# Performance work log

Measured on AMD Instinct MI355X. Metric: run time of the kernel, lower is better.

Reference implementation:

```python
import jax
import jax.numpy as jnp
import numpy as np

# --- dimensions ---
N, B, E, T = 16384, 64, 262144, 1048576   # atoms, molecules, edges, triplets
R, S = 128, 7                              # num_radial, num_spherical
A, EM, TR = 128, 256, 32                   # emb_size_atom, emb_size_edge, emb_size_trip
CRBF, C, BIL, L = 16, 16, 64, 2            # emb_size_rbf, emb_size_cbf, emb_size_bil_trip, num_blocks
NKR, DP = 128, 8                           # num_k_rbf, downprojection_size
CUTOFF, K_CUT, DK = 6.0, 0.4, 0.2


def _k_grid_np():
    ax = np.arange(-2, 3) * DK
    g = np.stack(np.meshgrid(ax, ax, ax, indexing='ij'), -1).reshape(-1, 3)
    nrm = np.linalg.norm(g, axis=1)
    return g[(nrm <= K_CUT + 1e-9) & (nrm > 1e-12)].astype(np.float32)  # [32,3]


def _k_rbf_np(kg):
    nrm = np.linalg.norm(kg, axis=1, keepdims=True)
    centers = np.linspace(0.0, K_CUT, NKR)[None, :]
    gamma = (NKR / K_CUT) ** 2
    return np.exp(-gamma * (nrm - centers) ** 2).astype(np.float32)  # [32,NKR]


def setup_inputs():
    key = jax.random.key(0)
    ks = iter(jax.random.split(key, 48))
    def nrm(shape, fan_in):
        return jax.random.normal(next(ks), shape, jnp.float32) * (fan_in ** -0.5)
    kg_np = _k_grid_np()
    apm = N // B  # atoms per molecule
    mol = jax.random.randint(next(ks), (E,), 0, B)
    inp = {
        'pos': jax.random.uniform(next(ks), (N, 3), jnp.float32) * 5.0,
        'atom_table': jax.random.normal(next(ks), (83, A), jnp.float32),
        'W_edge': nrm((2 * A + R, EM), 2 * A + R), 'b_edge': jnp.zeros((EM,), jnp.float32),
        'W_rbf3': nrm((R, CRBF), R), 'W_rbf3_E': nrm((L, CRBF, EM), CRBF),
        'W_cbf3': nrm((S, R, C), R),
        'W_ba': nrm((L, EM, EM), EM),
        'W_downtrip': nrm((L, EM, TR), EM),
        'W_bil': nrm((L, C, TR, BIL), C * TR),
        'W_up': nrm((L, BIL, EM), BIL),
        'W_res1': nrm((L, EM, EM), EM), 'W_res2': nrm((L, EM, EM), EM),
        'W_rbf_h': nrm((R, CRBF), R), 'W_h': nrm((L, CRBF, EM), CRBF),
        'W_atom': nrm((L, EM, A), EM),
        'k_grid': jnp.asarray(kg_np), 'k_rbf_values': jnp.asarray(_k_rbf_np(kg_np)),
        'W_downk': nrm((NKR, DP), NKR), 'W_kfilter': nrm((DP, A), DP),
        'W_ew': nrm((L, A, A), A),
        'W_cat': nrm((L, 2 * A + EM, EM), 2 * A + EM),
        'W_rbf_out': nrm((R, CRBF), R), 'W_oute': nrm((CRBF, EM), CRBF),
        'W_out1': nrm((EM, A), EM), 'W_out2': nrm((A, 1), A),
        'z': jax.random.randint(next(ks), (N,), 0, 83),
        'edge_src': mol * apm + jax.random.randint(next(ks), (E,), 0, apm),
        'edge_tgt': mol * apm + jax.random.randint(next(ks), (E,), 0, apm),
        'id3_ba': jax.random.randint(next(ks), (T,), 0, E),
        'id3_ca': jax.random.randint(next(ks), (T,), 0, E),
        'batch_idx': jnp.arange(N, dtype=jnp.int32) // apm,
    }
    return inp


def _legendre(x):
    # P_0..P_{S-1}(x) via recurrence
    p = [jnp.ones_like(x), x]
    for l in range(1, S - 1):
        p.append(((2 * l + 1) * x * p[-1] - l * p[-2]) / (l + 1))
    return jnp.stack(p[:S], axis=-1)  # [T,S]


def _forward(pos, atom_table, W_edge, b_edge, W_rbf3, W_rbf3_E, W_cbf3, W_ba,
             W_downtrip, W_bil, W_up, W_res1, W_res2, W_rbf_h, W_h, W_atom,
             k_grid, k_rbf_values, W_downk, W_kfilter, W_ew, W_cat,
             W_rbf_out, W_oute, W_out1, W_out2,
             z, edge_src, edge_tgt, id3_ba, id3_ca, batch_idx):
    seg = lambda x, ids, n: jax.ops.segment_sum(x, ids, num_segments=n)
    silu = jax.nn.silu
    isq2 = 2.0 ** -0.5

    # radial basis (spherical Bessel) with polynomial envelope p=5
    vec = pos[edge_src] - pos[edge_tgt]                       # [E,3]
    d = jnp.sqrt(jnp.sum(vec * vec, -1) + 1e-12)              # [E]
    ds = d / CUTOFF
    env = jnp.where(ds < 1.0, 1.0 - 21.0 * ds**5 + 35.0 * ds**6 - 15.0 * ds**7, 0.0)
    freq = jnp.arange(1, R + 1, dtype=pos.dtype) * jnp.pi
    rbf = env[:, None] * (2.0 / CUTOFF) ** 0.5 * jnp.sin(freq * ds[:, None]) / d[:, None]  # [E,R]

    # circular basis: Legendre polys of triplet angle b->a<-c, combined with rbf of edge c->a
    cos_ang = jnp.clip(jnp.sum(vec[id3_ba] * vec[id3_ca], -1) / (d[id3_ba] * d[id3_ca]), -1.0, 1.0)
    sph = _legendre(cos_ang)                                  # [T,S]
    rW = jnp.einsum('er,src->esc', rbf, W_cbf3)               # [E,S,C]
    cbf = jnp.zeros((sph.shape[0], C), pos.dtype)
    for s in range(S):  # small fixed loop over spherical order (memory-safe gather)
        cbf = cbf + sph[:, s, None] * rW[:, s, :][id3_ca]     # [T,C]

    # atom + edge embeddings
    h = atom_table[z]                                         # [N,A]
    m = silu(jnp.concatenate([h[edge_src], h[edge_tgt], rbf], -1) @ W_edge + b_edge)  # [E,EM]

    # Ewald k-space geometry and learned filter
    kdot = pos @ k_grid.T                                     # [N,K]
    cosk, sink = jnp.cos(kdot), jnp.sin(kdot)
    kf = silu(k_rbf_values @ W_downk) @ W_kfilter             # [K,A]

    for l in range(L):
        # triplet message passing: gather - bilinear with cbf - scatter
        rbf3e = (rbf @ W_rbf3) @ W_rbf3_E[l]                  # [E,EM]
        x_trip = silu((silu(m @ W_ba[l]) * rbf3e) @ W_downtrip[l])  # [E,TR]
        x_kj = x_trip[id3_ba]                                 # [T,TR]
        x3 = jnp.zeros((m.shape[0], BIL), m.dtype)
        for c in range(C):  # efficient bilinear, one cbf channel at a time
            x3 = x3 + seg(cbf[:, c, None] * x_kj, id3_ca, m.shape[0]) @ W_bil[l, c]
        m = (m + silu(x3 @ W_up[l])) * isq2
        m = (m + silu(silu(m @ W_res1[l]) @ W_res2[l])) * isq2
        # atom update: rbf-gated edge->atom scatter
        ha = seg(m * ((rbf @ W_rbf_h) @ W_h[l]), edge_tgt, h.shape[0]) @ W_atom[l]  # [N,A]
        # Ewald block: per-molecule structure factors, filtered in k-space
        sf_re = seg(cosk[:, :, None] * h[:, None, :], batch_idx, B) * kf  # [B,K,A]
        sf_im = seg(sink[:, :, None] * h[:, None, :], batch_idx, B) * kf
        ew = (jnp.einsum('nk,nka->na', cosk, sf_re[batch_idx]) +
              jnp.einsum('nk,nka->na', sink, sf_im[batch_idx]))           # [N,A]
        h = (h + silu(ha) + silu(ew @ W_ew[l])) * (3.0 ** -0.5)
        # edge refresh (concat block)
        m = silu(jnp.concatenate([h[edge_src], h[edge_tgt], m], -1) @ W_cat[l])

    # output block: rbf-gated scatter to atoms, per-molecule extensive energy
    Ea = seg(m * ((rbf @ W_rbf_out) @ W_oute), edge_tgt, h.shape[0])       # [N,EM]
    atom_e = silu(Ea @ W_out1) @ W_out2                                     # [N,1]
    return seg(atom_e[:, 0], batch_idx, B)                                  # [B]


def reference(pos, atom_table, W_edge, b_edge, W_rbf3, W_rbf3_E, W_cbf3, W_ba,
              W_downtrip, W_bil, W_up, W_res1, W_res2, W_rbf_h, W_h, W_atom,
              k_grid, k_rbf_values, W_downk, W_kfilter, W_ew, W_cat,
              W_rbf_out, W_oute, W_out1, W_out2,
              z, edge_src, edge_tgt, id3_ba, id3_ca, batch_idx):
    return _forward(pos, atom_table, W_edge, b_edge, W_rbf3, W_rbf3_E, W_cbf3, W_ba,
                    W_downtrip, W_bil, W_up, W_res1, W_res2, W_rbf_h, W_h, W_atom,
                    k_grid, k_rbf_values, W_downk, W_kfilter, W_ew, W_cat,
                    W_rbf_out, W_oute, W_out1, W_out2,
                    z, edge_src, edge_tgt, id3_ba, id3_ca, batch_idx)
```

## Files before the change

### kernel.cpp

```cpp
#include <hip/hip_runtime.h>
#include <math.h>

#define NA 16384
#define NB 64
#define NE 262144
#define NT 1048576
#define NR 128
#define DA 128
#define DEM 256
#define DTR 32
#define DC 16
#define DBIL 64
#define DNKR 128
#define DDP 8
#define NK 32
#define APM 256
#define PI_F 3.14159265358979323846f

typedef unsigned short u16;
typedef unsigned int u32;
typedef __attribute__((ext_vector_type(8))) short bf16x8;
typedef __attribute__((ext_vector_type(4))) float f32x4;

__device__ __forceinline__ float silu_f(float x){ return x / (1.0f + __expf(-x)); }
__device__ __forceinline__ float us2f(u32 u){ return __uint_as_float(u<<16); }
__device__ __forceinline__ u16 f2us(float f){
  u32 x = __float_as_uint(f);
  u32 r = x + 0x7fffu + ((x>>16)&1u);
  return (u16)(r>>16);
}
__device__ __forceinline__ void unp8(uint4 v, float* o){
  o[0]=us2f(v.x&0xffffu); o[1]=us2f(v.x>>16);
  o[2]=us2f(v.y&0xffffu); o[3]=us2f(v.y>>16);
  o[4]=us2f(v.z&0xffffu); o[5]=us2f(v.z>>16);
  o[6]=us2f(v.w&0xffffu); o[7]=us2f(v.w>>16);
}
__device__ __forceinline__ uint4 pack8(const float* v){
  uint4 r;
  r.x = (u32)f2us(v[0]) | ((u32)f2us(v[1])<<16);
  r.y = (u32)f2us(v[2]) | ((u32)f2us(v[3])<<16);
  r.z = (u32)f2us(v[4]) | ((u32)f2us(v[5])<<16);
  r.w = (u32)f2us(v[6]) | ((u32)f2us(v[7])<<16);
  return r;
}
__device__ __forceinline__ float rbf_val(float d, int r){
  float ds = d*(1.0f/6.0f);
  float env = 0.0f;
  if (ds < 1.0f){
    float p2 = ds*ds, p5 = p2*p2*ds;
    env = 1.0f - 21.0f*p5 + 35.0f*p5*ds - 15.0f*p5*p2;
  }
  return env * 0.5773502691896258f * __sinf((float)(r+1)*PI_F*ds) / d;
}

__device__ __forceinline__ bf16x8 ldsA(const u16* sA, int row, int KLD, int slot){
  int s = slot ^ (row&7);
  return *(const bf16x8*)(sA + row*KLD + s*8);
}
__device__ __forceinline__ void stSlot(u16* sA, int row, int KLD, int slot, uint4 v){
  int s = slot ^ (row&7);
  *(uint4*)(sA + row*KLD + s*8) = v;
}
__device__ __forceinline__ void stW(u16* sA, int row, int KLD, int col, u16 v){
  int s = (col>>3) ^ (row&7);
  sA[row*KLD + s*8 + (col&7)] = v;
}
__device__ __forceinline__ bf16x8 ldB(const u16* Wt, int col, int K, int koff){
  return *(const bf16x8*)(Wt + (size_t)col*K + koff);
}

__global__ void k_zero(int* __restrict__ p, int n){
  int i = blockIdx.x*256+threadIdx.x; if (i<n) p[i]=0;
}

__global__ void k_wprep(const float* __restrict__ src, u16* __restrict__ dst,
                        int K, int N, int Kpad){
  int i = blockIdx.x*256+threadIdx.x;
  if (i >= N*Kpad) return;
  int n = i / Kpad, k = i - n*Kpad;
  dst[(size_t)n*Kpad + k] = (k<K)? f2us(src[(size_t)k*N + n]) : (u16)0;
}
__global__ void k_wprep_cbf(const float* __restrict__ src, u16* __restrict__ dst){
  int i = blockIdx.x*256+threadIdx.x;
  if (i >= 112*128) return;
  int n = i>>7, k = i&127;
  int s = n>>4, c = n&15;
  dst[i] = f2us(src[s*2048 + k*16 + c]);
}

__global__ void k_iperm(const int* __restrict__ list, int n, int* __restrict__ iperm){
  int i = blockIdx.x*256+threadIdx.x;
  if (i<n) iperm[list[i]] = i;
}
__global__ void k_permute2(const int* __restrict__ list, const int* __restrict__ a,
                           const int* __restrict__ b, int n,
                           int* __restrict__ ap, int* __restrict__ bp){
  int i = blockIdx.x*256+threadIdx.x;
  if (i<n){ int e = list[i]; ap[i]=a[e]; bp[i]=b[e]; }
}
__global__ void k_count_map(const int* __restrict__ ids, const int* __restrict__ map,
                            int num, int* __restrict__ cnt){
  int i = blockIdx.x*256+threadIdx.x;
  if (i<num) atomicAdd(&cnt[map[ids[i]]],1);
}
__global__ void k_fill_valmap(const int* __restrict__ ids, const int* __restrict__ vals,
                              const int* __restrict__ map, int num,
                              int* __restrict__ cur, int* __restrict__ list){
  int i = blockIdx.x*256+threadIdx.x;
  if (i<num){ int p = atomicAdd(&cur[map[ids[i]]],1); list[p]=map[vals[i]]; }
}

__global__ void k_geom(const float* __restrict__ pos, const int* __restrict__ src,
                       const int* __restrict__ tgt, float4* __restrict__ vecd,
                       float* __restrict__ dlen){
  int e = blockIdx.x*256+threadIdx.x;
  if (e >= NE) return;
  int s = src[e], t = tgt[e];
  float vx = pos[s*3+0]-pos[t*3+0];
  float vy = pos[s*3+1]-pos[t*3+1];
  float vz = pos[s*3+2]-pos[t*3+2];
  float d = sqrtf(vx*vx+vy*vy+vz*vz + 1e-12f);
  vecd[e] = make_float4(vx,vy,vz,1.0f/d);
  dlen[e] = d;
}

__global__ void __launch_bounds__(256)
k_rbf16(const float* __restrict__ dlen, const float* __restrict__ W1,
        const float* __restrict__ W2, const float* __restrict__ W3,
        u16* __restrict__ r16a, u16* __restrict__ r16h, u16* __restrict__ r16o){
  __shared__ float rb[4*128];
  int e0 = blockIdx.x*4;
  int tid = threadIdx.x, eg = tid>>6, lt = tid&63;
  int e = e0+eg;
  float d = dlen[e];
  rb[eg*128+lt]    = rbf_val(d, lt);
  rb[eg*128+lt+64] = rbf_val(d, lt+64);
  __syncthreads();
  if (lt < 48){
    int which = lt>>4, jj = lt&15;
    const float* W = (which==0)? W1 : (which==1)? W2 : W3;
    float acc=0.f;
    for (int r=0;r<NR;r++) acc += rb[eg*128+r]*W[r*16+jj];
    u16* o = (which==0)? r16a : (which==1)? r16h : r16o;
    o[(size_t)e*16+jj] = f2us(acc);
  }
}

__global__ void k_gather_h(const float* __restrict__ table, const int* __restrict__ z,
                           float* __restrict__ h){
  int idx = blockIdx.x*256 + threadIdx.x;
  int n = idx >> 7, a = idx & 127;
  h[idx] = table[z[n]*DA + a];
}

__global__ void k_kdot(const float* __restrict__ pos, const float* __restrict__ kg,
                       float* __restrict__ cosk, float* __restrict__ sink_){
  int idx = blockIdx.x*256+threadIdx.x;
  int n = idx>>5, k = idx&31;
  float dotv = pos[n*3]*kg[k*3]+pos[n*3+1]*kg[k*3+1]+pos[n*3+2]*kg[k*3+2];
  float s, c;
  sincosf(dotv, &s, &c);
  cosk[idx] = c; sink_[idx] = s;
}

__global__ void k_kf(const float* __restrict__ krbf, const float* __restrict__ Wd,
                     const float* __restrict__ Wf, float* __restrict__ kf){
  __shared__ float t[NK*DDP];
  int tid = threadIdx.x;
  { int k = tid>>3, d = tid&7;
    float s=0.f;
    for (int r=0;r<DNKR;r++) s += krbf[k*DNKR+r]*Wd[r*DDP+d];
    t[tid] = silu_f(s); }
  __syncthreads();
  for (int idx=tid; idx<NK*DA; idx+=256){
    int k = idx>>7, a = idx&127;
    float s=0.f;
    #pragma unroll
    for (int d=0; d<DDP; d++) s += t[k*DDP+d]*Wf[d*DA+a];
    kf[idx]=s;
  }
}

__global__ void k_count(const int* __restrict__ ids, int num, int* __restrict__ cnt){
  int i = blockIdx.x*256+threadIdx.x;
  if (i<num) atomicAdd(&cnt[ids[i]],1);
}
__global__ void k_scan1(const int* __restrict__ cnt, int n, int* __restrict__ loc,
                        int* __restrict__ part){
  __shared__ int lds[256];
  int i = blockIdx.x*256+threadIdx.x;
  int v = (i<n)?cnt[i]:0;
  lds[threadIdx.x]=v; __syncthreads();
  for (int off=1; off<256; off<<=1){
    int tv = (threadIdx.x >= (unsigned)off)? lds[threadIdx.x-off]:0;
    __syncthreads();
    lds[threadIdx.x]+=tv;
    __syncthreads();
  }
  if (i<n) loc[i] = lds[threadIdx.x]-v;
  if (threadIdx.x==255) part[blockIdx.x]=lds[255];
}
__global__ void k_scan2(int* __restrict__ part, int nparts){
  __shared__ int lds[1024];
  int tid=threadIdx.x;
  for (int i=tid;i<1024;i+=256) lds[i] = (i<nparts)? part[i] : 0;
  __syncthreads();
  if (tid==0){
    int run=0;
    for (int i=0;i<nparts;i++){ int v=lds[i]; lds[i]=run; run+=v; }
  }
  __syncthreads();
  for (int i=tid;i<1024;i+=256) if (i<nparts) part[i]=lds[i];
}
__global__ void k_scan3(const int* __restrict__ loc, const int* __restrict__ part,
                        const int* __restrict__ cnt, int n, int* __restrict__ off){
  int i = blockIdx.x*256+threadIdx.x;
  if (i<n){ int o = loc[i]+part[i>>8]; off[i]=o; if (i==n-1) off[n]=o+cnt[i]; }
}
__global__ void k_copy_int(const int* __restrict__ a, int n, int* __restrict__ b){
  int i=blockIdx.x*256+threadIdx.x; if(i<n) b[i]=a[i];
}
__global__ void k_fill(const int* __restrict__ ids, int num, int* __restrict__ cur,
                       int* __restrict__ list){
  int i = blockIdx.x*256+threadIdx.x;
  if (i<num){ int p = atomicAdd(&cur[ids[i]],1); list[p]=i; }
}


__global__ void __launch_bounds__(256)
k_edgeinit_mx(const float* __restrict__ h, const float* __restrict__ dlen,
              const u16* __restrict__ Wt, const float* __restrict__ bias,
              const int* __restrict__ src, const int* __restrict__ tgt,
              u16* __restrict__ outm){
  __shared__ u16 sA[64*256];
  int e0 = blockIdx.x*64;
  int j = threadIdx.x, lane = j&63, w = j>>6;
  int rbase = (w&1)*32, cbase = (w>>1)*128;
  int l15 = lane&15, kg = lane>>4;
  f32x4 acc[2][8];
  #pragma unroll
  for (int rt=0;rt<2;rt++)
    #pragma unroll
    for (int i=0;i<8;i++) acc[rt][i] = (f32x4){0.f,0.f,0.f,0.f};
  for (int idx=j; idx<64*32; idx+=256){
    int row = idx>>5, slot = idx&31;
    int e = e0+row;
    const float* srcp = (slot<16)? (h + (size_t)src[e]*DA + slot*8)
                                 : (h + (size_t)tgt[e]*DA + (slot-16)*8);
    float v[8];
    float4 q0 = *(const float4*)srcp, q1 = *(const float4*)(srcp+4);
    v[0]=q0.x; v[1]=q0.y; v[2]=q0.z; v[3]=q0.w;
    v[4]=q1.x; v[5]=q1.y; v[6]=q1.z; v[7]=q1.w;
    stSlot(sA, row, 256, slot, pack8(v));
  }
  __syncthreads();
  #pragma unroll 2
  for (int kc=0; kc<8; kc++){
    bf16x8 a0 = ldsA(sA, rbase+l15,    256, kc*4+kg);
    bf16x8 a1 = ldsA(sA, rbase+16+l15, 256, kc*4+kg);
    #pragma unroll
    for (int ct=0; ct<8; ct++){
      bf16x8 b = ldB(Wt, cbase+ct*16+l15, 384, kc*32+kg*8);
      acc[0][ct] = __builtin_amdgcn_mfma_f32_16x16x32_bf16(a0, b, acc[0][ct], 0,0,0);
      acc[1][ct] = __builtin_amdgcn_mfma_f32_16x16x32_bf16(a1, b, acc[1][ct], 0,0,0);
    }
  }
  __syncthreads();
  for (int idx=j; idx<64*16; idx+=256){
    int row = idx>>4, slot = idx&15;
    float dv = dlen[e0+row];
    float v[8];
    #pragma unroll
    for (int q=0;q<8;q++) v[q] = rbf_val(dv, slot*8+q);
    stSlot(sA, row, 256, slot, pack8(v));
  }
  __syncthreads();
  #pragma unroll 2
  for (int kc=8; kc<12; kc++){
    bf16x8 a0 = ldsA(sA, rbase+l15,    256, (kc-8)*4+kg);
    bf16x8 a1 = ldsA(sA, rbase+16+l15, 256, (kc-8)*4+kg);
    #pragma unroll
    for (int ct=0; ct<8; ct++){
      bf16x8 b = ldB(Wt, cbase+ct*16+l15, 384, kc*32+kg*8);
      acc[0][ct] = __builtin_amdgcn_mfma_f32_16x16x32_bf16(a0, b, acc[0][ct], 0,0,0);
      acc[1][ct] = __builtin_amdgcn_mfma_f32_16x16x32_bf16(a1, b, acc[1][ct], 0,0,0);
    }
  }
  #pragma unroll
  for (int rt=0;rt<2;rt++)
  #pragma unroll
  for (int ct=0; ct<8; ct++){
    int col = cbase + ct*16 + l15;
    float bv = bias[col];
    #pragma unroll
    for (int r=0;r<4;r++){
      int row = rbase + rt*16 + kg*4 + r;
      outm[(size_t)(e0+row)*DEM + col] = f2us(silu_f(acc[rt][ct][r] + bv));
    }
  }
}

__global__ void __launch_bounds__(256)
k_ba_dt_mx(const u16* __restrict__ m, const u16* __restrict__ WtBA,
           const u16* __restrict__ r16, const u16* __restrict__ WtR3E,
           const u16* __restrict__ WtDT, u16* __restrict__ xtrip){
  __shared__ u16 sM[32*256];
  __shared__ u16 sR[32*64];
  int e0 = blockIdx.x*32;
  int j = threadIdx.x, lane = j&63, w = j>>6;
  for (int p=j; p<32*32; p+=256){
    int row = p>>5, slot = p&31;
    uint4 v = *(const uint4*)(m + (size_t)(e0+row)*DEM + slot*8);
    stSlot(sM, row, 256, slot, v);
  }
  for (int p=j; p<32*8; p+=256){
    int row = p>>3, slot = p&7;
    uint4 v = {0u,0u,0u,0u};
    if (slot<2) v = *(const uint4*)(r16 + (size_t)(e0+row)*16 + slot*8);
    stSlot(sR, row, 64, slot, v);
  }
  __syncthreads();
  int rbase = (w&1)*16, cbase = (w>>1)*128;
  int l15 = lane&15, kg = lane>>4;
  int arow = rbase + l15;
  f32x4 accA[8], accG[8];
  #pragma unroll
  for (int i=0;i<8;i++){ accA[i]=(f32x4){0.f,0.f,0.f,0.f}; accG[i]=(f32x4){0.f,0.f,0.f,0.f}; }
  #pragma unroll 2
  for (int kc=0; kc<8; kc++){
    bf16x8 a = ldsA(sM, arow, 256, kc*4+kg);
    #pragma unroll
    for (int ct=0; ct<8; ct++){
      bf16x8 b = ldB(WtBA, cbase+ct*16+l15, 256, kc*32+kg*8);
      accA[ct] = __builtin_amdgcn_mfma_f32_16x16x32_bf16(a, b, accA[ct], 0,0,0);
    }
  }
  { bf16x8 a = ldsA(sR, arow, 64, kg);
    #pragma unroll
    for (int ct=0; ct<8; ct++){
      bf16x8 b = ldB(WtR3E, cbase+ct*16+l15, 32, kg*8);
      accG[ct] = __builtin_amdgcn_mfma_f32_16x16x32_bf16(a, b, accG[ct], 0,0,0);
    } }
  __syncthreads();
  #pragma unroll
  for (int ct=0; ct<8; ct++){
    int col = cbase + ct*16 + l15;
    #pragma unroll
    for (int r=0;r<4;r++){
      int row = rbase + kg*4 + r;
      stW(sM, row, 256, col, f2us(silu_f(accA[ct][r])*accG[ct][r]));
    }
  }
  __syncthreads();
  int rb2 = (w&1)*16, ct2 = (w>>1);
  int arow2 = rb2 + l15;
  f32x4 acc2 = (f32x4){0.f,0.f,0.f,0.f};
  #pragma unroll 2
  for (int kc=0; kc<8; kc++){
    bf16x8 a = ldsA(sM, arow2, 256, kc*4+kg);
    bf16x8 b = ldB(WtDT, ct2*16+l15, 256, kc*32+kg*8);
    acc2 = __builtin_amdgcn_mfma_f32_16x16x32_bf16(a, b, acc2, 0,0,0);
  }
  #pragma unroll
  for (int r=0;r<4;r++){
    int row = rb2 + kg*4 + r;
    int col = ct2*16 + l15;
    xtrip[(size_t)(e0+row)*DTR + col] = f2us(silu_f(acc2[r]));
  }
}

__global__ void __launch_bounds__(256)
k_trip(const int* __restrict__ ca_off, const int* __restrict__ ba_list,
       const float4* __restrict__ vecd, const float* __restrict__ dlen,
       const u16* __restrict__ WtCBF, const u16* __restrict__ xtrip,
       const u16* __restrict__ WtBIL, const u16* __restrict__ WtUP,
       u16* __restrict__ m){
  __shared__ u16 sS3[16*512];
  __shared__ u16 sRB[16*128];
  __shared__ float rWl[16*112];
  __shared__ u16 sX3[16*64];
  int e0 = blockIdx.x*16;
  int tid = threadIdx.x, lane = tid&63, w = tid>>6;
  int l15 = lane&15, kg = lane>>4;
  for (int idx=tid; idx<2048; idx+=256){
    int e = idx>>7, r = idx&127;
    stW(sRB, e, 128, r, f2us(rbf_val(dlen[e0+e], r)));
  }
  __syncthreads();
  for (int ct=w; ct<7; ct+=4){
    f32x4 acc = (f32x4){0.f,0.f,0.f,0.f};
    for (int kc=0; kc<4; kc++){
      bf16x8 a = ldsA(sRB, l15, 128, kc*4+kg);
      bf16x8 b = ldB(WtCBF, ct*16+l15, 128, kc*32+kg*8);
      acc = __builtin_amdgcn_mfma_f32_16x16x32_bf16(a, b, acc, 0,0,0);
    }
    #pragma unroll
    for (int r=0;r<4;r++)
      rWl[(kg*4+r)*112 + ct*16 + l15] = acc[r];
  }
  __syncthreads();
  int half = lane>>5, tr = lane&31;
  for (int sub=0; sub<4; sub++){
    int el = w*4+sub, e = e0+el;
    float4 vd = vecd[e];
    float a0=0.f,a1=0.f,a2=0.f,a3=0.f,a4=0.f,a5=0.f,a6=0.f;
    int beg = ca_off[e], end = ca_off[e+1];
    int cnt = end - beg;
    int c0 = (cnt+1)>>1;
    int mybeg = beg + half*c0;
    int myend = half ? end : beg+c0;
    float4 bd = make_float4(0.f,0.f,0.f,1.f);
    float xk = 0.f;
    if (mybeg<myend){
      int b0 = ba_list[mybeg];
      bd = vecd[b0];
      xk = us2f(xtrip[(size_t)b0*DTR + tr]);
    }
    for (int ti=mybeg; ti<myend; ti++){
      int bn = (ti+1<myend)? ba_list[ti+1] : 0;
      float4 bd_n = vecd[bn];
      float xk_n = us2f(xtrip[(size_t)bn*DTR + tr]);
      float x = (vd.x*bd.x + vd.y*bd.y + vd.z*bd.z)*vd.w*bd.w;
      x = fminf(1.0f, fmaxf(-1.0f, x));
      float p2 = (3.f*x*x - 1.f)*0.5f;
      float p3 = (5.f*x*p2 - 2.f*x)*(1.0f/3.0f);
      float p4 = (7.f*x*p3 - 3.f*p2)*0.25f;
      float p5 = (9.f*x*p4 - 4.f*p3)*0.2f;
      float p6 = (11.f*x*p5 - 5.f*p4)*(1.0f/6.0f);
      a0 += xk;    a1 += x*xk;  a2 += p2*xk; a3 += p3*xk;
      a4 += p4*xk; a5 += p5*xk; a6 += p6*xk;
      bd = bd_n; xk = xk_n;
    }
    a0 += __shfl_xor(a0, 32); a1 += __shfl_xor(a1, 32);
    a2 += __shfl_xor(a2, 32); a3 += __shfl_xor(a3, 32);
    a4 += __shfl_xor(a4, 32); a5 += __shfl_xor(a5, 32);
    a6 += __shfl_xor(a6, 32);
    const float* rwe = rWl + el*112;
    #pragma unroll
    for (int q=0;q<8;q++){
      int c = half*8+q;
      float s3 = rwe[c]*a0 + rwe[16+c]*a1 + rwe[32+c]*a2 + rwe[48+c]*a3
               + rwe[64+c]*a4 + rwe[80+c]*a5 + rwe[96+c]*a6;
      stW(sS3, el, 512, c*32+tr, f2us(s3));
    }
  }
  __syncthreads();
  { f32x4 acc = (f32x4){0.f,0.f,0.f,0.f};
    #pragma unroll 2
    for (int kc=0; kc<16; kc++){
      bf16x8 a = ldsA(sS3, l15, 512, kc*4+kg);
      bf16x8 b = ldB(WtBIL, w*16+l15, 512, kc*32+kg*8);
      acc = __builtin_amdgcn_mfma_f32_16x16x32_bf16(a, b, acc, 0,0,0);
    }
    #pragma unroll
    for (int r=0;r<4;r++)
      stW(sX3, kg*4+r, 64, w*16+l15, f2us(acc[r]));
  }
  __syncthreads();
  f32x4 acc2[4];
  #pragma unroll
  for (int i=0;i<4;i++) acc2[i] = (f32x4){0.f,0.f,0.f,0.f};
  for (int kc=0; kc<2; kc++){
    bf16x8 a = ldsA(sX3, l15, 64, kc*4+kg);
    #pragma unroll
    for (int ct=0; ct<4; ct++){
      bf16x8 b = ldB(WtUP, w*64+ct*16+l15, 64, kc*32+kg*8);
      acc2[ct] = __builtin_amdgcn_mfma_f32_16x16x32_bf16(a, b, acc2[ct], 0,0,0);
    }
  }
  #pragma unroll
  for (int ct=0; ct<4; ct++){
    int col = w*64 + ct*16 + l15;
    #pragma unroll
    for (int r=0;r<4;r++){
      int row = kg*4 + r;
      size_t oi = (size_t)(e0+row)*DEM + col;
      m[oi] = f2us((us2f(m[oi]) + silu_f(acc2[ct][r]))*0.7071067811865476f);
    }
  }
}

__global__ void __launch_bounds__(256)
k_res_mx(const u16* __restrict__ WtR1, const u16* __restrict__ WtR2, u16* __restrict__ m){
  __shared__ u16 sM[64*256];
  int e0 = blockIdx.x*64;
  int j = threadIdx.x, lane = j&63, w = j>>6;
  for (int p=j; p<64*32; p+=256){
    int row = p>>5, slot = p&31;
    uint4 v = *(const uint4*)(m + (size_t)(e0+row)*DEM + slot*8);
    stSlot(sM, row, 256, slot, v);
  }
  __syncthreads();
  int rbase = (w&1)*32, cbase = (w>>1)*128;
  int l15 = lane&15, kg = lane>>4;
  f32x4 acc[2][8];
  #pragma unroll
  for (int rt=0;rt<2;rt++)
    #pragma unroll
    for (int i=0;i<8;i++) acc[rt][i]=(f32x4){0.f,0.f,0.f,0.f};
  #pragma unroll 2
  for (int kc=0; kc<8; kc++){
    bf16x8 a0 = ldsA(sM, rbase+l15,    256, kc*4+kg);
    bf16x8 a1 = ldsA(sM, rbase+16+l15, 256, kc*4+kg);
    #pragma unroll
    for (int ct=0; ct<8; ct++){
      bf16x8 b = ldB(WtR1, cbase+ct*16+l15, 256, kc*32+kg*8);
      acc[0][ct] = __builtin_amdgcn_mfma_f32_16x16x32_bf16(a0, b, acc[0][ct], 0,0,0);
      acc[1][ct] = __builtin_amdgcn_mfma_f32_16x16x32_bf16(a1, b, acc[1][ct], 0,0,0);
    }
  }
  __syncthreads();
  #pragma unroll
  for (int rt=0;rt<2;rt++)
  #pragma unroll
  for (int ct=0; ct<8; ct++){
    int col = cbase + ct*16 + l15;
    #pragma unroll
    for (int r=0;r<4;r++)
      stW(sM, rbase + rt*16 + kg*4 + r, 256, col, f2us(silu_f(acc[rt][ct][r])));
  }
  __syncthreads();
  #pragma unroll
  for (int rt=0;rt<2;rt++)
    #pragma unroll
    for (int i=0;i<8;i++) acc[rt][i]=(f32x4){0.f,0.f,0.f,0.f};
  #pragma unroll 2
  for (int kc=0; kc<8; kc++){
    bf16x8 a0 = ldsA(sM, rbase+l15,    256, kc*4+kg);
    bf16x8 a1 = ldsA(sM, rbase+16+l15, 256, kc*4+kg);
    #pragma unroll
    for (int ct=0; ct<8; ct++){
      bf16x8 b = ldB(WtR2, cbase+ct*16+l15, 256, kc*32+kg*8);
      acc[0][ct] = __builtin_amdgcn_mfma_f32_16x16x32_bf16(a0, b, acc[0][ct], 0,0,0);
      acc[1][ct] = __builtin_amdgcn_mfma_f32_16x16x32_bf16(a1, b, acc[1][ct], 0,0,0);
    }
  }
  #pragma unroll
  for (int rt=0;rt<2;rt++)
  #pragma unroll
  for (int ct=0; ct<8; ct++){
    int col = cbase + ct*16 + l15;
    #pragma unroll
    for (int r=0;r<4;r++){
      int row = rbase + rt*16 + kg*4 + r;
      size_t oi = (size_t)(e0+row)*DEM + col;
      float orig = us2f(m[oi]);
      m[oi] = f2us((orig + silu_f(acc[rt][ct][r]))*0.7071067811865476f);
    }
  }
}

__global__ void __launch_bounds__(256)
k_catref_mx(const float* __restrict__ h, const u16* __restrict__ Wt,
            const int* __restrict__ src, const int* __restrict__ tgt,
            u16* __restrict__ m){
  __shared__ u16 sA[64*256];
  int e0 = blockIdx.x*64;
  int j = threadIdx.x, lane = j&63, w = j>>6;
  int rbase = (w&1)*32, cbase = (w>>1)*128;
  int l15 = lane&15, kg = lane>>4;
  f32x4 acc[2][8];
  #pragma unroll
  for (int rt=0;rt<2;rt++)
    #pragma unroll
    for (int i=0;i<8;i++) acc[rt][i]=(f32x4){0.f,0.f,0.f,0.f};
  for (int idx=j; idx<64*32; idx+=256){
    int row = idx>>5, slot = idx&31;
    int e = e0+row;
    const float* srcp = (slot<16)? (h + (size_t)src[e]*DA + slot*8)
                                 : (h + (size_t)tgt[e]*DA + (slot-16)*8);
    float v[8];
    float4 q0 = *(const float4*)srcp, q1 = *(const float4*)(srcp+4);
    v[0]=q0.x; v[1]=q0.y; v[2]=q0.z; v[3]=q0.w;
    v[4]=q1.x; v[5]=q1.y; v[6]=q1.z; v[7]=q1.w;
    stSlot(sA, row, 256, slot, pack8(v));
  }
  __syncthreads();
  #pragma unroll 2
  for (int kc=0; kc<8; kc++){
    bf16x8 a0 = ldsA(sA, rbase+l15,    256, kc*4+kg);
    bf16x8 a1 = ldsA(sA, rbase+16+l15, 256, kc*4+kg);
    #pragma unroll
    for (int ct=0; ct<8; ct++){
      bf16x8 b = ldB(Wt, cbase+ct*16+l15, 512, kc*32+kg*8);
      acc[0][ct] = __builtin_amdgcn_mfma_f32_16x16x32_bf16(a0, b, acc[0][ct], 0,0,0);
      acc[1][ct] = __builtin_amdgcn_mfma_f32_16x16x32_bf16(a1, b, acc[1][ct], 0,0,0);
    }
  }
  __syncthreads();
  for (int p=j; p<64*32; p+=256){
    int row = p>>5, slot = p&31;
    uint4 v = *(const uint4*)(m + (size_t)(e0+row)*DEM + slot*8);
    stSlot(sA, row, 256, slot, v);
  }
  __syncthreads();
  #pragma unroll 2
  for (int kc=8; kc<16; kc++){
    bf16x8 a0 = ldsA(sA, rbase+l15,    256, (kc-8)*4+kg);
    bf16x8 a1 = ldsA(sA, rbase+16+l15, 256, (kc-8)*4+kg);
    #pragma unroll
    for (int ct=0; ct<8; ct++){
      bf16x8 b = ldB(Wt, cbase+ct*16+l15, 512, kc*32+kg*8);
      acc[0][ct] = __builtin_amdgcn_mfma_f32_16x16x32_bf16(a0, b, acc[0][ct], 0,0,0);
      acc[1][ct] = __builtin_amdgcn_mfma_f32_16x16x32_bf16(a1, b, acc[1][ct], 0,0,0);
    }
  }
  __syncthreads();
  #pragma unroll
  for (int rt=0;rt<2;rt++)
  #pragma unroll
  for (int ct=0; ct<8; ct++){
    int col = cbase + ct*16 + l15;
    #pragma unroll
    for (int r=0;r<4;r++){
      int row = rbase + rt*16 + kg*4 + r;
      m[(size_t)(e0+row)*DEM + col] = f2us(silu_f(acc[rt][ct][r]));
    }
  }
}

__global__ void __launch_bounds__(256)
k_gseg_seq(const int* __restrict__ off, const u16* __restrict__ m,
           const u16* __restrict__ r16, const float* __restrict__ Wg,
           float* __restrict__ outp){
  __shared__ float sW[16*256];
  int n = blockIdx.x, j = threadIdx.x;
  for (int idx=j; idx<4096; idx+=256) sW[idx] = Wg[idx];
  __syncthreads();
  float s = 0.f;
  int beg = off[n], end = off[n+1];
  for (int e=beg; e<end; e++){
    const uint4* rp = (const uint4*)(r16 + (size_t)e*16);
    float rv[16];
    unp8(rp[0], rv); unp8(rp[1], rv+8);
    float g = 0.f;
    #pragma unroll
    for (int i=0;i<16;i++) g += rv[i]*sW[i*256+j];
    s += us2f(m[(size_t)e*DEM + j])*g;
  }
  outp[(size_t)n*DEM + j] = s;
}

__global__ void k_sf(const float* __restrict__ cosk, const float* __restrict__ sink_,
                     const float* __restrict__ h, const float* __restrict__ kf,
                     float* __restrict__ sfre, float* __restrict__ sfim){
  int bk = blockIdx.x; int b = bk>>5, k = bk&31;
  int a = threadIdx.x;
  float sre=0.f, sim=0.f;
  int n0 = b*APM;
  for (int i=0;i<APM;i++){
    float c = cosk[(n0+i)*NK+k];
    float s = sink_[(n0+i)*NK+k];
    float hv = h[(size_t)(n0+i)*DA+a];
    sre += c*hv; sim += s*hv;
  }
  float f = kf[k*DA+a];
  sfre[(size_t)bk*DA+a] = sre*f;
  sfim[(size_t)bk*DA+a] = sim*f;
}

__global__ void k_ew(const float* __restrict__ cosk, const float* __restrict__ sink_,
                     const float* __restrict__ sfre, const float* __restrict__ sfim,
                     float* __restrict__ ew){
  int n = blockIdx.x; int a = threadIdx.x; int b = n>>8;
  float s=0.f;
  for (int k=0;k<NK;k++){
    s += cosk[n*NK+k]*sfre[(size_t)(b*NK+k)*DA+a] + sink_[n*NK+k]*sfim[(size_t)(b*NK+k)*DA+a];
  }
  ew[(size_t)n*DA+a]=s;
}

__global__ void __launch_bounds__(128)
k_hup(const float* __restrict__ hsum, const float* __restrict__ ewb,
      const float* __restrict__ Wat, const float* __restrict__ Wew,
      float* __restrict__ h){
  __shared__ float sA[16*256];
  __shared__ float sB[16*128];
  int row0 = blockIdx.x*16;
  int j = threadIdx.x;
  for (int idx=j; idx<4096; idx+=128) sA[idx] = hsum[(size_t)row0*DEM + idx];
  for (int idx=j; idx<2048; idx+=128) sB[idx] = ewb[(size_t)row0*DA + idx];
  __syncthreads();
  float a1[16], a2[16];
  #pragma unroll
  for (int i=0;i<16;i++){ a1[i]=0.f; a2[i]=0.f; }
  for (int k=0;k<256;k++){
    float w = Wat[k*DA+j];
    #pragma unroll
    for (int i=0;i<16;i++) a1[i] += sA[i*256+k]*w;
  }
  for (int k=0;k<128;k++){
    float w = Wew[k*DA+j];
    #pragma unroll
    for (int i=0;i<16;i++) a2[i] += sB[i*128+k]*w;
  }
  #pragma unroll
  for (int i=0;i<16;i++){
    size_t oi = (size_t)(row0+i)*DA + j;
    h[oi] = (h[oi] + silu_f(a1[i]) + silu_f(a2[i]))*0.5773502691896258f;
  }
}

__global__ void k_out_atom(const float* __restrict__ Ea, const float* __restrict__ W1,
                           const float* __restrict__ W2, float* __restrict__ atom_e){
  __shared__ float red[128];
  int n = blockIdx.x; int j = threadIdx.x;
  const float* row = Ea + (size_t)n*DEM;
  float s=0.f;
  for (int k=0;k<DEM;k++) s += row[k]*W1[k*DA+j];
  float v = silu_f(s)*W2[j];
  red[j]=v; __syncthreads();
  for (int st=64; st>0; st>>=1){ if (j<st) red[j]+=red[j+st]; __syncthreads(); }
  if (j==0) atom_e[n]=red[0];
}

__global__ void k_out_mol(const float* __restrict__ atom_e, float* __restrict__ out){
  __shared__ float red[256];
  int b = blockIdx.x; int t = threadIdx.x;
  red[t] = atom_e[b*APM+t]; __syncthreads();
  for (int st=128; st>0; st>>=1){ if (t<st) red[t]+=red[t+st]; __syncthreads(); }
  if (t==0) out[b]=red[0];
}

extern "C" void kernel_launch(void* const* d_in, const int* in_sizes, int n_in,
                              void* d_out, int out_size, void* d_ws, size_t ws_size,
                              hipStream_t stream){
  (void)in_sizes; (void)n_in; (void)out_size;
  const float* pos    = (const float*)d_in[0];
  const float* atab   = (const float*)d_in[1];
  const float* W_edge = (const float*)d_in[2];
  const float* b_edge = (const float*)d_in[3];
  const float* W_rbf3 = (const float*)d_in[4];
  const float* W_rbf3E= (const float*)d_in[5];
  const float* W_cbf3 = (const float*)d_in[6];
  const float* W_ba   = (const float*)d_in[7];
  const float* W_dt   = (const float*)d_in[8];
  const float* W_bil  = (const float*)d_in[9];
  const float* W_up   = (const float*)d_in[10];
  const float* W_r1   = (const float*)d_in[11];
  const float* W_r2   = (const float*)d_in[12];
  const float* W_rbfh = (const float*)d_in[13];
  const float* W_h    = (const float*)d_in[14];
  const float* W_atom = (const float*)d_in[15];
  const float* kgrid  = (const float*)d_in[16];
  const float* krbfv  = (const float*)d_in[17];
  const float* W_dk   = (const float*)d_in[18];
  const float* W_kf   = (const float*)d_in[19];
  const float* W_ewm  = (const float*)d_in[20];
  const float* W_cat  = (const float*)d_in[21];
  const float* W_rbfo = (const float*)d_in[22];
  const float* W_oute = (const float*)d_in[23];
  const float* W_o1   = (const float*)d_in[24];
  const float* W_o2   = (const float*)d_in[25];
  const int* z     = (const int*)d_in[26];
  const int* esrc  = (const int*)d_in[27];
  const int* etgt  = (const int*)d_in[28];
  const int* id3ba = (const int*)d_in[29];
  const int* id3ca = (const int*)d_in[30];
  float* out = (float*)d_out;

  char* base = (char*)d_ws;
  size_t off = 0;
  auto alloc = [&](size_t bytes)->char*{
    char* p = base + off;
    off += (bytes + 255) & ~(size_t)255;
    return p;
  };
  u16*   m     = (u16*)  alloc((size_t)NE*DEM*2);
  float4* vecd = (float4*)alloc((size_t)NE*16);
  float* dlen  = (float*)alloc((size_t)NE*4);
  u16*   r16a  = (u16*)  alloc((size_t)NE*16*2);
  u16*   r16h  = (u16*)  alloc((size_t)NE*16*2);
  u16*   r16o  = (u16*)  alloc((size_t)NE*16*2);
  float* h     = (float*)alloc((size_t)NA*DA*4);
  float* cosk  = (float*)alloc((size_t)NA*NK*4);
  float* sinkb = (float*)alloc((size_t)NA*NK*4);
  float* sfre  = (float*)alloc((size_t)NB*NK*DA*4);
  float* sfim  = (float*)alloc((size_t)NB*NK*DA*4);
  float* kf    = (float*)alloc((size_t)NK*DA*4);
  float* atome = (float*)alloc((size_t)NA*4);
  char*  scr   = alloc((size_t)24*1024*1024);
  int* tgt_off = (int*)alloc((size_t)(NA+1)*4);
  int* tgt_list= (int*)alloc((size_t)NE*4);
  int* iperm   = (int*)alloc((size_t)NE*4);
  int* esrc_p  = (int*)alloc((size_t)NE*4);
  int* etgt_p  = (int*)alloc((size_t)NE*4);
  int* ca_off  = (int*)alloc((size_t)(NE+1)*4);
  int* ca_list = (int*)alloc((size_t)NT*4);
  int* parts   = (int*)alloc((size_t)1024*4);
  u16* wt_edge = (u16*)alloc((size_t)256*384*2);
  u16* wt_ba   = (u16*)alloc((size_t)2*256*256*2);
  u16* wt_r3e  = (u16*)alloc((size_t)2*256*32*2);
  u16* wt_dt   = (u16*)alloc((size_t)2*32*256*2);
  u16* wt_up   = (u16*)alloc((size_t)2*256*64*2);
  u16* wt_r1   = (u16*)alloc((size_t)2*256*256*2);
  u16* wt_r2   = (u16*)alloc((size_t)2*256*256*2);
  u16* wt_cat  = (u16*)alloc((size_t)2*256*512*2);
  u16* wt_cbf  = (u16*)alloc((size_t)112*128*2);
  u16* wt_bil  = (u16*)alloc((size_t)2*64*512*2);
  size_t need = off;
  if (ws_size < need) return;

  u16*   xtrip = (u16*)scr;
  float* hsum  = (float*)scr;
  float* ewb   = (float*)(scr + (size_t)16*1024*1024);
  int* tmpi    = (int*)r16a;
  int* tgt_cnt = tmpi;
  int* tgt_loc = tmpi + NA;
  int* tgt_cur = tmpi + 2*NA;
  int* ca_cnt  = tmpi + 3*NA;
  int* ca_loc  = ca_cnt + NE;
  int* ca_cur  = ca_loc + NE;

  auto wprep = [&](const float* src, u16* dst, int K, int N, int Kpad){
    int tot = N*Kpad;
    k_wprep<<<(tot+255)/256, 256, 0, stream>>>(src, dst, K, N, Kpad);
  };
  wprep(W_edge, wt_edge, 384, 256, 384);
  k_wprep_cbf<<<(112*128+255)/256, 256, 0, stream>>>(W_cbf3, wt_cbf);
  for (int l=0; l<2; l++){
    wprep(W_ba  + (size_t)l*256*256, wt_ba  + (size_t)l*256*256, 256, 256, 256);
    wprep(W_rbf3E+(size_t)l*16*256,  wt_r3e + (size_t)l*256*32,  16,  256, 32);
    wprep(W_dt  + (size_t)l*256*32,  wt_dt  + (size_t)l*32*256,  256, 32,  256);
    wprep(W_up  + (size_t)l*64*256,  wt_up  + (size_t)l*256*64,  64,  256, 64);
    wprep(W_r1  + (size_t)l*256*256, wt_r1  + (size_t)l*256*256, 256, 256, 256);
    wprep(W_r2  + (size_t)l*256*256, wt_r2  + (size_t)l*256*256, 256, 256, 256);
    wprep(W_cat + (size_t)l*512*256, wt_cat + (size_t)l*256*512, 512, 256, 512);
    wprep(W_bil + (size_t)l*512*64,  wt_bil + (size_t)l*64*512,  512, 64,  512);
  }

  k_zero<<<NA/256, 256, 0, stream>>>(tgt_cnt, NA);
  k_count<<<NE/256, 256, 0, stream>>>(etgt, NE, tgt_cnt);
  k_scan1<<<NA/256, 256, 0, stream>>>(tgt_cnt, NA, tgt_loc, parts);
  k_scan2<<<1, 256, 0, stream>>>(parts, NA/256);
  k_scan3<<<NA/256, 256, 0, stream>>>(tgt_loc, parts, tgt_cnt, NA, tgt_off);
  k_copy_int<<<NA/256, 256, 0, stream>>>(tgt_off, NA, tgt_cur);
  k_fill<<<NE/256, 256, 0, stream>>>(etgt, NE, tgt_cur, tgt_list);
  k_iperm<<<NE/256, 256, 0, stream>>>(tgt_list, NE, iperm);
  k_permute2<<<NE/256, 256, 0, stream>>>(tgt_list, esrc, etgt, NE, esrc_p, etgt_p);

  k_geom<<<NE/256, 256, 0, stream>>>(pos, esrc_p, etgt_p, vecd, dlen);

  k_zero<<<NE/256, 256, 0, stream>>>(ca_cnt, NE);
  k_count_map<<<NT/256, 256, 0, stream>>>(id3ca, iperm, NT, ca_cnt);
  k_scan1<<<NE/256, 256, 0, stream>>>(ca_cnt, NE, ca_loc, parts);
  k_scan2<<<1, 256, 0, stream>>>(parts, NE/256);
  k_scan3<<<NE/256, 256, 0, stream>>>(ca_loc, parts, ca_cnt, NE, ca_off);
  k_copy_int<<<NE/256, 256, 0, stream>>>(ca_off, NE, ca_cur);
  k_fill_valmap<<<NT/256, 256, 0, stream>>>(id3ca, id3ba, iperm, NT, ca_cur, ca_list);

  k_rbf16<<<NE/4, 256, 0, stream>>>(dlen, W_rbf3, W_rbfh, W_rbfo, r16a, r16h, r16o);
  k_gather_h<<<NA*DA/256, 256, 0, stream>>>(atab, z, h);
  k_kdot<<<NA*NK/256, 256, 0, stream>>>(pos, kgrid, cosk, sinkb);
  k_kf<<<1, 256, 0, stream>>>(krbfv, W_dk, W_kf, kf);
  k_edgeinit_mx<<<NE/64, 256, 0, stream>>>(h, dlen, wt_edge, b_edge, esrc_p, etgt_p, m);

  for (int l=0; l<2; l++){
    k_ba_dt_mx<<<NE/32, 256, 0, stream>>>(m, wt_ba + (size_t)l*256*256,
                                          r16a, wt_r3e + (size_t)l*256*32,
                                          wt_dt + (size_t)l*32*256, xtrip);
    k_trip<<<NE/16, 256, 0, stream>>>(ca_off, ca_list, vecd, dlen, wt_cbf,
                                      xtrip, wt_bil + (size_t)l*64*512,
                                      wt_up + (size_t)l*256*64, m);
    k_res_mx<<<NE/64, 256, 0, stream>>>(wt_r1 + (size_t)l*256*256,
                                        wt_r2 + (size_t)l*256*256, m);
    k_gseg_seq<<<NA, 256, 0, stream>>>(tgt_off, m, r16h, W_h + (size_t)l*16*DEM, hsum);
    k_sf<<<NB*NK, 128, 0, stream>>>(cosk, sinkb, h, kf, sfre, sfim);
    k_ew<<<NA, 128, 0, stream>>>(cosk, sinkb, sfre, sfim, ewb);
    k_hup<<<NA/16, 128, 0, stream>>>(hsum, ewb, W_atom + (size_t)l*DEM*DA,
                                     W_ewm + (size_t)l*DA*DA, h);
    k_catref_mx<<<NE/64, 256, 0, stream>>>(h, wt_cat + (size_t)l*256*512, esrc_p, etgt_p, m);
  }

  k_gseg_seq<<<NA, 256, 0, stream>>>(tgt_off, m, r16o, W_oute, hsum);
  k_out_atom<<<NA, 128, 0, stream>>>(hsum, W_o1, W_o2, atome);
  k_out_mol<<<NB, 256, 0, stream>>>(atome, out);
}
```

Baseline: 3.819 ms.

## Batch weight-prep launches and dual-stream the triplet gather loop

```diff
diff --git a/kernel.cpp b/kernel.cpp
--- a/kernel.cpp
+++ b/kernel.cpp
@@ -73,12 +73,22 @@
   int i = blockIdx.x*256+threadIdx.x; if (i<n) p[i]=0;
 }
 
-__global__ void k_wprep(const float* __restrict__ src, u16* __restrict__ dst,
-                        int K, int N, int Kpad){
-  int i = blockIdx.x*256+threadIdx.x;
-  if (i >= N*Kpad) return;
-  int n = i / Kpad, k = i - n*Kpad;
-  dst[(size_t)n*Kpad + k] = (k<K)? f2us(src[(size_t)k*N + n]) : (u16)0;
+struct WprepDesc { const float* src; u16* dst; int K; int N; int Kpad; int elems; };
+struct WprepTable { WprepDesc d[15]; int n; };
+__global__ void k_wprep_all(WprepTable t){
+  long long i = (long long)blockIdx.x*256 + threadIdx.x;
+  for (int q=0;q<15;q++){
+    if (q >= t.n) return;
+    int e = t.d[q].elems;
+    if (i < e){
+      int Kpad = t.d[q].Kpad;
+      int n = (int)(i / Kpad), k = (int)(i - (long long)n*Kpad);
+      t.d[q].dst[(size_t)n*Kpad + k] =
+        (k < t.d[q].K)? f2us(t.d[q].src[(size_t)k*t.d[q].N + n]) : (u16)0;
+      return;
+    }
+    i -= e;
+  }
 }
 __global__ void k_wprep_cbf(const float* __restrict__ src, u16* __restrict__ dst){
   int i = blockIdx.x*256+threadIdx.x;
@@ -409,27 +419,55 @@
     int c0 = (cnt+1)>>1;
     int mybeg = beg + half*c0;
     int myend = half ? end : beg+c0;
-    float4 bd = make_float4(0.f,0.f,0.f,1.f);
-    float xk = 0.f;
-    if (mybeg<myend){
+    int len = myend - mybeg;
+    int nA = (len+1)>>1;
+    int aEnd = mybeg + nA;
+    float4 bdA = make_float4(0.f,0.f,0.f,1.f), bdB = make_float4(0.f,0.f,0.f,1.f);
+    float xkA = 0.f, xkB = 0.f;
+    if (len > 0){
       int b0 = ba_list[mybeg];
-      bd = vecd[b0];
-      xk = us2f(xtrip[(size_t)b0*DTR + tr]);
-    }
-    for (int ti=mybeg; ti<myend; ti++){
-      int bn = (ti+1<myend)? ba_list[ti+1] : 0;
-      float4 bd_n = vecd[bn];
-      float xk_n = us2f(xtrip[(size_t)bn*DTR + tr]);
-      float x = (vd.x*bd.x + vd.y*bd.y + vd.z*bd.z)*vd.w*bd.w;
-      x = fminf(1.0f, fmaxf(-1.0f, x));
-      float p2 = (3.f*x*x - 1.f)*0.5f;
-      float p3 = (5.f*x*p2 - 2.f*x)*(1.0f/3.0f);
-      float p4 = (7.f*x*p3 - 3.f*p2)*0.25f;
-      float p5 = (9.f*x*p4 - 4.f*p3)*0.2f;
-      float p6 = (11.f*x*p5 - 5.f*p4)*(1.0f/6.0f);
-      a0 += xk;    a1 += x*xk;  a2 += p2*xk; a3 += p3*xk;
-      a4 += p4*xk; a5 += p5*xk; a6 += p6*xk;
-      bd = bd_n; xk = xk_n;
+      bdA = vecd[b0];
+      xkA = us2f(xtrip[(size_t)b0*DTR + tr]);
+    }
+    if (aEnd < myend){
+      int b0 = ba_list[aEnd];
+      bdB = vecd[b0];
+      xkB = us2f(xtrip[(size_t)b0*DTR + tr]);
+    }
+    for (int i=0; i<nA; i++){
+      int tiA = mybeg + i;
+      int bnA = (tiA+1<aEnd)? ba_list[tiA+1] : 0;
+      float4 bdA_n = vecd[bnA];
+      float xkA_n = us2f(xtrip[(size_t)bnA*DTR + tr]);
+      int tiB = aEnd + i;
+      bool vB = tiB < myend;
+      int bnB = (tiB+1<myend)? ba_list[tiB+1] : 0;
+      float4 bdB_n = vecd[bnB];
+      float xkB_n = us2f(xtrip[(size_t)bnB*DTR + tr]);
+      {
+        float x = (vd.x*bdA.x + vd.y*bdA.y + vd.z*bdA.z)*vd.w*bdA.w;
+        x = fminf(1.0f, fmaxf(-1.0f, x));
+        float p2 = (3.f*x*x - 1.f)*0.5f;
+        float p3 = (5.f*x*p2 - 2.f*x)*(1.0f/3.0f);
+        float p4 = (7.f*x*p3 - 3.f*p2)*0.25f;
+        float p5 = (9.f*x*p4 - 4.f*p3)*0.2f;
+        float p6 = (11.f*x*p5 - 5.f*p4)*(1.0f/6.0f);
+        a0 += xkA;    a1 += x*xkA;  a2 += p2*xkA; a3 += p3*xkA;
+        a4 += p4*xkA; a5 += p5*xkA; a6 += p6*xkA;
+      }
+      if (vB){
+        float x = (vd.x*bdB.x + vd.y*bdB.y + vd.z*bdB.z)*vd.w*bdB.w;
+        x = fminf(1.0f, fmaxf(-1.0f, x));
+        float p2 = (3.f*x*x - 1.f)*0.5f;
+        float p3 = (5.f*x*p2 - 2.f*x)*(1.0f/3.0f);
+        float p4 = (7.f*x*p3 - 3.f*p2)*0.25f;
+        float p5 = (9.f*x*p4 - 4.f*p3)*0.2f;
+        float p6 = (11.f*x*p5 - 5.f*p4)*(1.0f/6.0f);
+        a0 += xkB;    a1 += x*xkB;  a2 += p2*xkB; a3 += p3*xkB;
+        a4 += p4*xkB; a5 += p5*xkB; a6 += p6*xkB;
+      }
+      bdA = bdA_n; xkA = xkA_n;
+      bdB = bdB_n; xkB = xkB_n;
     }
     a0 += __shfl_xor(a0, 32); a1 += __shfl_xor(a1, 32);
     a2 += __shfl_xor(a2, 32); a3 += __shfl_xor(a3, 32);
@@ -812,22 +850,40 @@
   int* ca_loc  = ca_cnt + NE;
   int* ca_cur  = ca_loc + NE;
 
-  auto wprep = [&](const float* src, u16* dst, int K, int N, int Kpad){
-    int tot = N*Kpad;
-    k_wprep<<<(tot+255)/256, 256, 0, stream>>>(src, dst, K, N, Kpad);
+  WprepTable wt;
+  int wn = 0;
+  auto addw = [&](const float* src, u16* dst, int K, int N, int Kpad){
+    wt.d[wn].src = src; wt.d[wn].dst = dst; wt.d[wn].K = K; wt.d[wn].N = N;
+    wt.d[wn].Kpad = Kpad; wt.d[wn].elems = N*Kpad; wn++;
   };
-  wprep(W_edge, wt_edge, 384, 256, 384);
+  addw(W_edge, wt_edge, 384, 256, 384);
+  for (int l=0; l<2; l++){
+    addw(W_ba  + (size_t)l*256*256, wt_ba  + (size_t)l*256*256, 256, 256, 256);
+    addw(W_rbf3E+(size_t)l*16*256,  wt_r3e + (size_t)l*256*32,  16,  256, 32);
+    addw(W_dt  + (size_t)l*256*32,  wt_dt  + (size_t)l*32*256,  256, 32,  256);
+    addw(W_up  + (size_t)l*64*256,  wt_up  + (size_t)l*256*64,  64,  256, 64);
+    addw(W_r1  + (size_t)l*256*256, wt_r1  + (size_t)l*256*256, 256, 256, 256);
+    addw(W_r2  + (size_t)l*256*256, wt_r2  + (size_t)l*256*256, 256, 256, 256);
+    addw(W_cat + (size_t)l*512*256, wt_cat + (size_t)l*256*512, 512, 256, 512);
+  }
+  wt.n = wn;
+  long long wtot = 0;
+  for (int q=0;q<wn;q++) wtot += wt.d[q].elems;
+  k_wprep_all<<<(int)((wtot+255)/256), 256, 0, stream>>>(wt);
+  {
+    WprepTable wb; int bn=0;
+    auto addb = [&](const float* src, u16* dst, int K, int N, int Kpad){
+      wb.d[bn].src=src; wb.d[bn].dst=dst; wb.d[bn].K=K; wb.d[bn].N=N;
+      wb.d[bn].Kpad=Kpad; wb.d[bn].elems=N*Kpad; bn++;
+    };
+    addb(W_bil, wt_bil, 512, 64, 512);
+    addb(W_bil + (size_t)512*64, wt_bil + (size_t)64*512, 512, 64, 512);
+    wb.n = bn;
+    long long btot = 0;
+    for (int q=0;q<bn;q++) btot += wb.d[q].elems;
+    k_wprep_all<<<(int)((btot+255)/256), 256, 0, stream>>>(wb);
+  }
   k_wprep_cbf<<<(112*128+255)/256, 256, 0, stream>>>(W_cbf3, wt_cbf);
-  for (int l=0; l<2; l++){
-    wprep(W_ba  + (size_t)l*256*256, wt_ba  + (size_t)l*256*256, 256, 256, 256);
-    wprep(W_rbf3E+(size_t)l*16*256,  wt_r3e + (size_t)l*256*32,  16,  256, 32);
-    wprep(W_dt  + (size_t)l*256*32,  wt_dt  + (size_t)l*32*256,  256, 32,  256);
-    wprep(W_up  + (size_t)l*64*256,  wt_up  + (size_t)l*256*64,  64,  256, 64);
-    wprep(W_r1  + (size_t)l*256*256, wt_r1  + (size_t)l*256*256, 256, 256, 256);
-    wprep(W_r2  + (size_t)l*256*256, wt_r2  + (size_t)l*256*256, 256, 256, 256);
-    wprep(W_cat + (size_t)l*512*256, wt_cat + (size_t)l*256*512, 512, 256, 512);
-    wprep(W_bil + (size_t)l*512*64,  wt_bil + (size_t)l*64*512,  512, 64,  512);
-  }
 
   k_zero<<<NA/256, 256, 0, stream>>>(tgt_cnt, NA);
   k_count<<<NE/256, 256, 0, stream>>>(etgt, NE, tgt_cnt);
```

Result: no change. 3.862 ms (+1.1%).
